# Kernel optimization log

Hardware: AMD Instinct MI355X
Metric: run time of the kernel (lower is better)

The kernel has to match this reference:

```python
import jax, jax.numpy as jnp
import numpy as np


def setup_inputs() -> dict:
    key = jax.random.key(0)
    ks = jax.random.split(key, 6)
    B, S, D, L = 4, 4096, 1024, 8192
    return {
        "inputs": jax.random.normal(ks[0], (B, S, D), dtype=jnp.float32),
        "W_w": jax.random.normal(ks[1], (D, D), dtype=jnp.float32) * (1.0 / np.sqrt(D)),
        "W_b": jax.random.normal(ks[2], (D,), dtype=jnp.float32) * 0.02,
        "U_w": jax.random.normal(ks[3], (L, D), dtype=jnp.float32) * (1.0 / np.sqrt(D)),
        "final_w": jax.random.normal(ks[4], (L, D), dtype=jnp.float32) * (1.0 / np.sqrt(D)),
        "final_b": jax.random.normal(ks[5], (L,), dtype=jnp.float32) * 0.02,
    }


def reference(inputs, W_w, W_b, U_w, final_w, final_b):
    # Z = tanh(W(inputs)): [B,S,D]
    Z = jnp.tanh(jnp.einsum("bsd,ed->bse", inputs, W_w) + W_b)
    # scores = U.weight @ Z^T: [B,L,S], softmax over seq
    scores = jnp.einsum("ld,bsd->bls", U_w, Z)
    alpha = jax.nn.softmax(scores, axis=2)
    # hidden = alpha @ inputs: [B,L,D]
    hidden = jnp.einsum("bls,bsd->bld", alpha, inputs)
    # logits = sum_d final_w[l,d]*hidden[b,l,d] + final_b[l]: [B,L]
    logits = jnp.einsum("ld,bld->bl", final_w, hidden) + final_b
    return logits
```

## Files before the change

### kernel.cpp

```cpp
#include <hip/hip_runtime.h>

typedef __attribute__((ext_vector_type(8))) short bf16x8;
typedef __attribute__((ext_vector_type(4))) float f32x4;
typedef unsigned short us;

#define DEVINL __device__ __forceinline__
#define AS1 __attribute__((address_space(1)))
#define AS3 __attribute__((address_space(3)))

constexpr int BB = 4, SS = 4096, DD = 1024, LL = 8192;
constexpr int LT_ = 128;
constexpr int STB = 256;
constexpr int BK  = 32;
constexpr int NST = SS / STB;
constexpr int KST = DD / BK;
constexpr int NU  = NST * KST;
constexpr int U_SH = LT_ * BK;
constexpr int Z_SH = STB * BK;
constexpr int SLOT_SH = 2*U_SH + 2*Z_SH;
constexpr int ZKST = DD / 64;

DEVINL unsigned short f2bf(float f){
  union { float f; unsigned u; } a; a.f = f;
  unsigned r = a.u + 0x7fffu + ((a.u >> 16) & 1u);
  return (unsigned short)(r >> 16);
}

DEVINL void gll16(const void* src, void* dst){
  __builtin_amdgcn_global_load_lds((const AS1 unsigned int*)src,
                                   (AS3 unsigned int*)dst, 16, 0, 0);
}

__global__ void conv_kernel(const float4* __restrict__ in,
                            ushort4* __restrict__ out, int n4){
  int stride = gridDim.x * blockDim.x;
  for (int i = blockIdx.x*blockDim.x + threadIdx.x; i < n4; i += stride){
    float4 v = in[i];
    ushort4 o;
    o.x = f2bf(v.x); o.y = f2bf(v.y); o.z = f2bf(v.z); o.w = f2bf(v.w);
    out[i] = o;
  }
}

constexpr int ZTILE = 128 * 64;

DEVINL bf16x8 zread_frag(const us* tile, int row, int chunk){
  return *(const AS3 bf16x8*)(tile + row*64 + ((chunk ^ (row & 7)) << 3));
}

DEVINL void stage_tile128(const us* __restrict__ g0, int row0, int d0,
                          us* ldsbase, int wave, int lane){
#pragma unroll
  for (int it = 0; it < 4; ++it){
    int off  = it*4096 + wave*1024 + lane*16;
    int row  = off >> 7;
    int slot = (off >> 4) & 7;
    int scol = (slot ^ (row & 7)) << 3;
    gll16(g0 + (size_t)(row0 + row) * DD + d0 + scol,
          ldsbase + ((it*4096 + wave*1024) >> 1));
  }
}

__global__ __launch_bounds__(256, 2) void zgemm_kernel(
    const us* __restrict__ X, const us* __restrict__ W,
    const float* __restrict__ Wb, us* __restrict__ Z)
{
  __shared__ __align__(16) us lds[2*ZTILE];
  const int bid = blockIdx.x;
  const int tm = bid & 127;
  const int tn = bid >> 7;
  const int tid = threadIdx.x, wave = tid >> 6, lane = tid & 63;
  const int wl = wave >> 1, wn = wave & 1;
  const int g = lane >> 4, cc = lane & 15;

  f32x4 acc[4][4] = {};
#pragma unroll 1
  for (int ks = 0; ks < ZKST; ++ks){
    __syncthreads();
    stage_tile128(X, tm*128, ks*64, lds,         wave, lane);
    stage_tile128(W, tn*128, ks*64, lds + ZTILE, wave, lane);
    __syncthreads();
#pragma unroll
    for (int ksub = 0; ksub < 2; ++ksub){
      bf16x8 af[4], bfr[4];
#pragma unroll
      for (int f = 0; f < 4; ++f) af[f]  = zread_frag(lds,         wl*64 + f*16 + cc, ksub*4 + g);
#pragma unroll
      for (int f = 0; f < 4; ++f) bfr[f] = zread_frag(lds + ZTILE, wn*64 + f*16 + cc, ksub*4 + g);
#pragma unroll
      for (int fm = 0; fm < 4; ++fm)
#pragma unroll
        for (int fn = 0; fn < 4; ++fn)
          acc[fm][fn] = __builtin_amdgcn_mfma_f32_16x16x32_bf16(af[fm], bfr[fn], acc[fm][fn], 0, 0, 0);
    }
  }
#pragma unroll
  for (int fm = 0; fm < 4; ++fm)
#pragma unroll
    for (int fn = 0; fn < 4; ++fn)
#pragma unroll
      for (int r = 0; r < 4; ++r){
        int row = tm*128 + wl*64 + fm*16 + 4*g + r;
        int col = tn*128 + wn*64 + fn*16 + cc;
        float y = acc[fm][fn][r] + Wb[col];
        float e2 = __expf(2.f * y);
        float t = 1.f - 2.f / (e2 + 1.f);
        Z[(size_t)row*DD + col] = f2bf(t);
      }
}

__global__ __launch_bounds__(512, 2) void fused_kernel(
    const us* __restrict__ U, const us* __restrict__ F,
    const us* __restrict__ Z, const us* __restrict__ X,
    float* __restrict__ pse, float* __restrict__ pac)
{
  __shared__ __align__(16) us lds[3 * SLOT_SH];

  const int h = blockIdx.x;
  const int xcd = h & 7, j = h >> 3;
  const int lt = xcd * 8 + (j & 7);
  const int b  = j >> 3;

  const int tid = threadIdx.x;
  const int wave = tid >> 6, lane = tid & 63;
  const int wl = wave >> 2, ws = wave & 3;
  const int g = lane >> 4, cc = lane & 15;

  const us* Ub = U + (size_t)lt * LT_ * DD;
  const us* Fb = F + (size_t)lt * LT_ * DD;
  const us* Zb = Z + (size_t)b * SS * DD;
  const us* Xb = X + (size_t)b * SS * DD;

  const int lg   = ((tid & 3) - (tid >> 3)) & 3;
  const int offA = (tid >> 2) * DD + lg * 8;

  const int sl8 = ((g + (cc >> 1)) & 3) * 8;

  f32x4 sacc[4][4] = {}, gacc[4][4] = {};
  float se_pk = 0.f, ac_pk = 0.f;

  auto stage_unit = [&](int n){
    int nn = (n >= NU) ? n - NU : n;
    us* sb = lds + (n % 3) * SLOT_SH;
    const int k32 = (nn & 31) * BK;
    const size_t stoff = (size_t)(nn >> 5) * STB * DD;
    gll16(Ub + k32 + offA, sb + tid*8);
    gll16(Fb + k32 + offA, sb + U_SH + tid*8);
    const us* pZ = Zb + stoff + k32 + offA;
    gll16(pZ,          sb + 2*U_SH + tid*8);
    gll16(pZ + 128*DD, sb + 2*U_SH + 4096 + tid*8);
    const us* pX = Xb + stoff + k32 + offA;
    gll16(pX,          sb + 2*U_SH + Z_SH + tid*8);
    gll16(pX + 128*DD, sb + 2*U_SH + Z_SH + 4096 + tid*8);
  };

  stage_unit(0);
  stage_unit(1);

#pragma unroll 1
  for (int u = 0; u < NU; ++u){
    asm volatile("s_waitcnt vmcnt(6)" ::: "memory");
    __builtin_amdgcn_s_barrier();
    stage_unit(u + 2);

    const us* sb = lds + (u % 3) * SLOT_SH;
    const us* tU = sb;
    const us* tF = sb + U_SH;
    const us* tZ = sb + 2*U_SH;
    const us* tX = sb + 2*U_SH + Z_SH;

    bf16x8 a0[4], b0[4], a1[4], b1[4];
#pragma unroll
    for (int f = 0; f < 4; ++f)
      a0[f] = *(const AS3 bf16x8*)(tU + (wl*64 + f*16 + cc)*BK + sl8);
#pragma unroll
    for (int f = 0; f < 4; ++f)
      b0[f] = *(const AS3 bf16x8*)(tZ + (ws*64 + f*16 + cc)*BK + sl8);
    __builtin_amdgcn_s_setprio(1);
#pragma unroll
    for (int fm = 0; fm < 4; ++fm)
#pragma unroll
      for (int fn = 0; fn < 4; ++fn)
        sacc[fm][fn] = __builtin_amdgcn_mfma_f32_16x16x32_bf16(a0[fm], b0[fn], sacc[fm][fn], 0, 0, 0);
    __builtin_amdgcn_s_setprio(0);

#pragma unroll
    for (int f = 0; f < 4; ++f)
      a1[f] = *(const AS3 bf16x8*)(tF + (wl*64 + f*16 + cc)*BK + sl8);
#pragma unroll
    for (int f = 0; f < 4; ++f)
      b1[f] = *(const AS3 bf16x8*)(tX + (ws*64 + f*16 + cc)*BK + sl8);
    __builtin_amdgcn_s_setprio(1);
#pragma unroll
    for (int fm = 0; fm < 4; ++fm)
#pragma unroll
      for (int fn = 0; fn < 4; ++fn)
        gacc[fm][fn] = __builtin_amdgcn_mfma_f32_16x16x32_bf16(a1[fm], b1[fn], gacc[fm][fn], 0, 0, 0);
    __builtin_amdgcn_s_setprio(0);

    if ((u & 31) == 31){
#pragma unroll
      for (int fm = 0; fm < 4; ++fm)
#pragma unroll
        for (int r = 0; r < 4; ++r){
          float ps = 0.f, pg = 0.f;
#pragma unroll
          for (int fn = 0; fn < 4; ++fn){
            float p = __expf(sacc[fm][fn][r]);
            ps += p;
            pg += p * gacc[fm][fn][r];
          }
#pragma unroll
          for (int m = 1; m < 16; m <<= 1){
            ps += __shfl_xor(ps, m, 64);
            pg += __shfl_xor(pg, m, 64);
          }
          bool sel = (cc == fm*4 + r);
          se_pk += sel ? ps : 0.f;
          ac_pk += sel ? pg : 0.f;
        }
#pragma unroll
      for (int fm = 0; fm < 4; ++fm)
#pragma unroll
        for (int fn = 0; fn < 4; ++fn){
          sacc[fm][fn] = f32x4{0.f, 0.f, 0.f, 0.f};
          gacc[fm][fn] = f32x4{0.f, 0.f, 0.f, 0.f};
        }
    }
  }

  {
    int row = (cc >> 2)*16 + 4*g + (cc & 3);
    int l = lt*LT_ + wl*64 + row;
    size_t idx = ((size_t)b*LL + l)*4 + ws;
    pse[idx] = se_pk;
    pac[idx] = ac_pk;
  }
}

__global__ void combine_kernel(const float* __restrict__ pse, const float* __restrict__ pac,
                               const float* __restrict__ fb, float* __restrict__ out)
{
  int i = blockIdx.x*blockDim.x + threadIdx.x;
  if (i >= BB*LL) return;
  int l = i & (LL - 1);
  float s = 0.f, a = 0.f;
#pragma unroll
  for (int k = 0; k < 4; ++k){
    s += pse[(size_t)i*4 + k];
    a += pac[(size_t)i*4 + k];
  }
  out[i] = a / s + fb[l];
}

extern "C" void kernel_launch(void* const* d_in, const int* in_sizes, int n_in,
                              void* d_out, int out_size, void* d_ws, size_t ws_size,
                              hipStream_t stream)
{
  const float* inp = (const float*)d_in[0];
  const float* Ww  = (const float*)d_in[1];
  const float* Wb  = (const float*)d_in[2];
  const float* Uw  = (const float*)d_in[3];
  const float* Fw  = (const float*)d_in[4];
  const float* fb  = (const float*)d_in[5];
  float* out = (float*)d_out;

  char* ws = (char*)d_ws;
  us* Xbf = (us*)(ws);
  us* Zbf = (us*)(ws + (size_t)32*1024*1024);
  us* Ubf = (us*)(ws + (size_t)64*1024*1024);
  us* Fbf = (us*)(ws + (size_t)80*1024*1024);
  us* Wbf = (us*)(ws + (size_t)96*1024*1024);
  float* pse = (float*)(ws + (size_t)98*1024*1024);
  float* pac = (float*)(ws + (size_t)99*1024*1024);

  conv_kernel<<<2048, 256, 0, stream>>>((const float4*)inp, (ushort4*)Xbf, BB*SS*DD/4);
  conv_kernel<<<256,  256, 0, stream>>>((const float4*)Ww,  (ushort4*)Wbf, DD*DD/4);
  conv_kernel<<<1024, 256, 0, stream>>>((const float4*)Uw,  (ushort4*)Ubf, LL*DD/4);
  conv_kernel<<<1024, 256, 0, stream>>>((const float4*)Fw,  (ushort4*)Fbf, LL*DD/4);

  zgemm_kernel<<<128*8, 256, 0, stream>>>(Xbf, Wbf, Wb, Zbf);
  fused_kernel<<<256, 512, 0, stream>>>(Ubf, Fbf, Zbf, Xbf, pse, pac);
  combine_kernel<<<(BB*LL + 255)/256, 256, 0, stream>>>(pse, pac, fb, out);
}
```

Baseline: 645.8 us.

## Prefetch next unit's U/Z fragments into registers and move barrier after MFMAs

Restructures the main loop so the U and Z LDS fragments for the next unit are loaded into registers at the end of the current iteration. The score MFMAs can then start right away, while the F and X fragment reads are still in flight. Global staging now runs three units ahead: the wait and barrier move after the MFMA blocks, and sched_barriers pin the instruction order. This adds 32 VGPRs of live prefetch registers, which may reduce occupancy.

```diff
diff --git a/kernel.cpp b/kernel.cpp
--- a/kernel.cpp
+++ b/kernel.cpp
@@ -135,6 +135,9 @@
   const int offA = (tid >> 2) * DD + lg * 8;
 
   const int sl8 = ((g + (cc >> 1)) & 3) * 8;
+
+  const int arow = (wl*64 + cc) * BK + sl8;
+  const int brow = (ws*64 + cc) * BK + sl8;
 
   f32x4 sacc[4][4] = {}, gacc[4][4] = {};
   float se_pk = 0.f, ac_pk = 0.f;
@@ -156,40 +159,41 @@
 
   stage_unit(0);
   stage_unit(1);
+  stage_unit(2);
+  asm volatile("s_waitcnt vmcnt(12)" ::: "memory");
+  __builtin_amdgcn_s_barrier();
+
+  bf16x8 pa[4], pb[4];
+#pragma unroll
+  for (int f = 0; f < 4; ++f)
+    pa[f] = *(const AS3 bf16x8*)(lds + arow + f*16*BK);
+#pragma unroll
+  for (int f = 0; f < 4; ++f)
+    pb[f] = *(const AS3 bf16x8*)(lds + 2*U_SH + brow + f*16*BK);
 
 #pragma unroll 1
   for (int u = 0; u < NU; ++u){
-    asm volatile("s_waitcnt vmcnt(6)" ::: "memory");
-    __builtin_amdgcn_s_barrier();
-    stage_unit(u + 2);
-
     const us* sb = lds + (u % 3) * SLOT_SH;
-    const us* tU = sb;
     const us* tF = sb + U_SH;
-    const us* tZ = sb + 2*U_SH;
     const us* tX = sb + 2*U_SH + Z_SH;
 
-    bf16x8 a0[4], b0[4], a1[4], b1[4];
+    bf16x8 a1[4], b1[4];
 #pragma unroll
     for (int f = 0; f < 4; ++f)
-      a0[f] = *(const AS3 bf16x8*)(tU + (wl*64 + f*16 + cc)*BK + sl8);
+      a1[f] = *(const AS3 bf16x8*)(tF + arow + f*16*BK);
 #pragma unroll
     for (int f = 0; f < 4; ++f)
-      b0[f] = *(const AS3 bf16x8*)(tZ + (ws*64 + f*16 + cc)*BK + sl8);
+      b1[f] = *(const AS3 bf16x8*)(tX + brow + f*16*BK);
+    __builtin_amdgcn_sched_barrier(0);
+
     __builtin_amdgcn_s_setprio(1);
 #pragma unroll
     for (int fm = 0; fm < 4; ++fm)
 #pragma unroll
       for (int fn = 0; fn < 4; ++fn)
-        sacc[fm][fn] = __builtin_amdgcn_mfma_f32_16x16x32_bf16(a0[fm], b0[fn], sacc[fm][fn], 0, 0, 0);
+        sacc[fm][fn] = __builtin_amdgcn_mfma_f32_16x16x32_bf16(pa[fm], pb[fn], sacc[fm][fn], 0, 0, 0);
     __builtin_amdgcn_s_setprio(0);
 
-#pragma unroll
-    for (int f = 0; f < 4; ++f)
-      a1[f] = *(const AS3 bf16x8*)(tF + (wl*64 + f*16 + cc)*BK + sl8);
-#pragma unroll
-    for (int f = 0; f < 4; ++f)
-      b1[f] = *(const AS3 bf16x8*)(tX + (ws*64 + f*16 + cc)*BK + sl8);
     __builtin_amdgcn_s_setprio(1);
 #pragma unroll
     for (int fm = 0; fm < 4; ++fm)
@@ -197,6 +201,22 @@
       for (int fn = 0; fn < 4; ++fn)
         gacc[fm][fn] = __builtin_amdgcn_mfma_f32_16x16x32_bf16(a1[fm], b1[fn], gacc[fm][fn], 0, 0, 0);
     __builtin_amdgcn_s_setprio(0);
+
+    asm volatile("s_waitcnt vmcnt(6)" ::: "memory");
+    __builtin_amdgcn_s_barrier();
+    stage_unit(u + 3);
+
+    {
+      int un = u + 1; if (un >= NU) un -= NU;
+      const us* sn = lds + (un % 3) * SLOT_SH;
+#pragma unroll
+      for (int f = 0; f < 4; ++f)
+        pa[f] = *(const AS3 bf16x8*)(sn + arow + f*16*BK);
+#pragma unroll
+      for (int f = 0; f < 4; ++f)
+        pb[f] = *(const AS3 bf16x8*)(sn + 2*U_SH + brow + f*16*BK);
+    }
+    __builtin_amdgcn_sched_barrier(0);
 
     if ((u & 31) == 31){
 #pragma unroll
```

Result: faster. 632.3 us (-2.1%).
